# Kernel tuning notes

Measured on AMD Instinct MI355X. Metric: run time of the kernel, lower is better.

The kernel has to match this reference:

```python
import jax, jax.numpy as jnp
import numpy as np

N_QUBITS = 4
N_LAYERS = 2
_I2 = jnp.eye(2, dtype=jnp.complex64)
_X = jnp.array([[0.0, 1.0], [1.0, 0.0]], dtype=jnp.complex64)


def _apply_1q_batched(state, U, wire):
    # state: [B,2,2,2,2] complex, U: [B,2,2] (per-sample gate)
    s = jnp.moveaxis(state, 1 + wire, -1)
    s = jnp.einsum('bij,b...j->b...i', U, s)
    return jnp.moveaxis(s, -1, 1 + wire)


def _apply_1q(state, U, wire):
    # shared 2x2 gate on `wire`
    s = jnp.moveaxis(state, 1 + wire, -1)
    s = jnp.einsum('ij,...j->...i', U, s)
    return jnp.moveaxis(s, -1, 1 + wire)


def _apply_cnot(state, c, t):
    s = jnp.moveaxis(state, (1 + c, 1 + t), (-2, -1))  # [...,2(ctrl),2(tgt)]
    s = jnp.stack([s[..., 0, :], s[..., 1, ::-1]], axis=-2)  # flip target if ctrl=1
    return jnp.moveaxis(s, (-2, -1), (1 + c, 1 + t))


def _rot_matrix(phi, theta, omega):
    # qml.Rot = RZ(omega) @ RY(theta) @ RZ(phi)
    c, s = jnp.cos(theta / 2), jnp.sin(theta / 2)
    ep = jnp.exp(-0.5j * (phi + omega))  # e^{-i(phi+omega)/2}
    em = jnp.exp(-0.5j * (phi - omega))  # e^{-i(phi-omega)/2}
    return jnp.stack([
        jnp.stack([ep * c, -jnp.conj(em) * s]),
        jnp.stack([em * s, jnp.conj(ep) * c]),
    ]).astype(jnp.complex64)


def _circuit(angles, weights):
    # angles: [B, 4] real; weights: [2, 4, 3] real -> [B, 4] PauliZ expvals
    B = angles.shape[0]
    state = jnp.zeros((B,) + (2,) * N_QUBITS, jnp.complex64)
    state = state.at[(slice(None),) + (0,) * N_QUBITS].set(1.0)  # |0000>
    # AngleEmbedding (rotation='X'): RX(angle_w) on wire w, batched over samples
    for w in range(N_QUBITS):
        half = angles[:, w] / 2
        c, s = jnp.cos(half), jnp.sin(half)
        U = c[:, None, None] * _I2 - 1j * s[:, None, None] * _X  # [B,2,2]
        state = _apply_1q_batched(state, U, w)
    # StronglyEntanglingLayers: Rot on each wire, then ring of CNOTs with range r
    for l in range(N_LAYERS):
        for w in range(N_QUBITS):
            U = _rot_matrix(weights[l, w, 0], weights[l, w, 1], weights[l, w, 2])
            state = _apply_1q(state, U, w)
        r = (l % (N_QUBITS - 1)) + 1  # PennyLane default ranges
        for w in range(N_QUBITS):
            state = _apply_cnot(state, w, (w + r) % N_QUBITS)
    probs = state.real ** 2 + state.imag ** 2  # [B,2,2,2,2]
    z = []
    for w in range(N_QUBITS):
        other = tuple(a for a in range(1, N_QUBITS + 1) if a != 1 + w)
        p = probs.sum(other)  # [B,2]
        z.append(p[:, 0] - p[:, 1])
    return jnp.stack(z, axis=-1)  # [B,4]


def setup_inputs() -> dict:
    key = jax.random.key(0)
    ks = jax.random.split(key, 6)
    B, D_IN, D_OUT, NQ = 65536, 512, 512, N_QUBITS
    x = jax.random.normal(ks[0], (B, D_IN), jnp.float32)
    pre_W = jax.random.normal(ks[1], (NQ, D_IN), jnp.float32) / np.sqrt(D_IN)
    pre_b = jax.random.normal(ks[2], (NQ,), jnp.float32) * 0.05
    weights = jax.random.uniform(ks[3], (N_LAYERS, NQ, 3), jnp.float32) * (2 * np.pi)
    post_W = jax.random.normal(ks[4], (D_OUT, NQ), jnp.float32) / np.sqrt(NQ)
    post_b = jax.random.normal(ks[5], (D_OUT,), jnp.float32) * 0.05
    return {"x": x, "pre_W": pre_W, "pre_b": pre_b, "weights": weights,
            "post_W": post_W, "post_b": post_b}


def reference(x, pre_W, pre_b, weights, post_W, post_b):
    angles = jnp.tanh(x @ pre_W.T + pre_b) * jnp.pi  # [B,4]
    q = _circuit(angles, weights)                    # [B,4]
    return q @ post_W.T + post_b                     # [B,512]
```

## Files before the change

### kernel.cpp

```cpp
#include <hip/hip_runtime.h>
#include <math.h>

#define PI_F 3.14159265358979323846f


typedef float floatx4 __attribute__((ext_vector_type(4)));

static __device__ __forceinline__ void st_store4(float* p, floatx4 v)
{
    *reinterpret_cast<floatx4*>(p) = v;
}

static __device__ __forceinline__ float fast_tanh(float a)
{
    a = fminf(fmaxf(a, -15.f), 15.f);
    const float e = __expf(2.f * a);
    return (e - 1.f) / (e + 1.f);
}

template<int ST>
__device__ __forceinline__ void rot_inlane(float* ar, float* ai,
    float u00r, float u00i, float u01r, float u01i,
    float u10r, float u10i, float u11r, float u11i)
{
#pragma unroll
    for (int k = 0; k < 4; ++k) {
        if (k & ST) continue;
        const int j = k | ST;
        const float Ar = ar[k], Ai = ai[k], Br = ar[j], Bi = ai[j];
        ar[k] = u00r*Ar - u00i*Ai + u01r*Br - u01i*Bi;
        ai[k] = u00r*Ai + u00i*Ar + u01r*Bi + u01i*Br;
        ar[j] = u10r*Ar - u10i*Ai + u11r*Br - u11i*Bi;
        ai[j] = u10r*Ai + u10i*Ar + u11r*Bi + u11i*Br;
    }
}

template<int XM>
__device__ __forceinline__ void rot_cross(float* ar, float* ai, bool ownB,
    float u00r, float u00i, float u01r, float u01i,
    float u10r, float u10i, float u11r, float u11i)
{
    const float cAr = ownB ? u11r : u00r;
    const float cAi = ownB ? u11i : u00i;
    const float cBr = ownB ? u10r : u01r;
    const float cBi = ownB ? u10i : u01i;
#pragma unroll
    for (int k = 0; k < 4; ++k) {
        const float pr = __shfl_xor(ar[k], XM, 64);
        const float pi = __shfl_xor(ai[k], XM, 64);
        const float vr = ar[k], vi = ai[k];
        ar[k] = cAr*vr - cAi*vi + cBr*pr - cBi*pi;
        ai[k] = cAr*vi + cAi*vr + cBr*pi + cBi*pr;
    }
}

#define ROT_COEFFS(L, W) \
    const float ph = wts[((L)*4+(W))*3+0]; \
    const float th = wts[((L)*4+(W))*3+1]; \
    const float om = wts[((L)*4+(W))*3+2]; \
    const float s_  = __sinf(0.5f*th),        c_  = __cosf(0.5f*th); \
    const float sp_ = __sinf(0.5f*(ph+om)),   cp_ = __cosf(0.5f*(ph+om)); \
    const float sq_ = __sinf(0.5f*(ph-om)),   cq_ = __cosf(0.5f*(ph-om));

#define U_ARGS cp_*c_, -sp_*c_, -cq_*s_, -sq_*s_, cq_*s_, -sq_*s_, cp_*c_, sp_*c_

__global__ __launch_bounds__(256) void k_fused(
    const float* __restrict__ x,
    const float* __restrict__ preW,
    const float* __restrict__ preb,
    const float* __restrict__ wts,
    const float* __restrict__ postW,
    const float* __restrict__ postb,
    float* __restrict__ out, int B)
{
    const int lane  = threadIdx.x & 63;
    const int wid   = threadIdx.x >> 6;
    const int base  = blockIdx.x * 64;
    const int wbase = base + wid * 16;
    if (base >= B) return;

    __shared__ float4 angLds[64];

    float4 wA[4], wB[4];
#pragma unroll
    for (int w = 0; w < 4; ++w) {
        wA[w] = *reinterpret_cast<const float4*>(preW + w * 512 + lane * 4);
        wB[w] = *reinterpret_cast<const float4*>(preW + w * 512 + 256 + lane * 4);
    }
    const float4 pb = *reinterpret_cast<const float4*>(preb);

#pragma unroll
    for (int p = 0; p < 4; ++p) {
        const int b0 = wbase + p * 4;

        float4 xa[4], xb[4];
#pragma unroll
        for (int t = 0; t < 4; ++t) {
            const float* xr = x + (size_t)(b0 + t) * 512;
            xa[t] = *reinterpret_cast<const float4*>(xr + lane * 4);
            xb[t] = *reinterpret_cast<const float4*>(xr + 256 + lane * 4);
        }

        float acc[4][4];
#pragma unroll
        for (int t = 0; t < 4; ++t) {
#pragma unroll
            for (int w = 0; w < 4; ++w) {
                acc[t][w] = xa[t].x * wA[w].x + xa[t].y * wA[w].y + xa[t].z * wA[w].z + xa[t].w * wA[w].w
                          + xb[t].x * wB[w].x + xb[t].y * wB[w].y + xb[t].z * wB[w].z + xb[t].w * wB[w].w;
            }
        }

        float v[4];
#pragma unroll
        for (int t = 0; t < 4; ++t) {
            float a01 = (lane & 1) ? acc[t][1] : acc[t][0];
            float b01 = (lane & 1) ? acc[t][0] : acc[t][1];
            a01 += __shfl_xor(b01, 1, 64);
            float a23 = (lane & 1) ? acc[t][3] : acc[t][2];
            float b23 = (lane & 1) ? acc[t][2] : acc[t][3];
            a23 += __shfl_xor(b23, 1, 64);
            const float vv = (lane & 2) ? a23 : a01;
            const float uu = (lane & 2) ? a01 : a23;
            v[t] = vv + __shfl_xor(uu, 2, 64);
        }
        float c01 = (lane & 4) ? v[1] : v[0];
        float d01 = (lane & 4) ? v[0] : v[1];
        c01 += __shfl_xor(d01, 4, 64);
        float c23 = (lane & 4) ? v[3] : v[2];
        float d23 = (lane & 4) ? v[2] : v[3];
        c23 += __shfl_xor(d23, 4, 64);
        float m = (lane & 8) ? c23 : c01;
        float n = (lane & 8) ? c01 : c23;
        m += __shfl_xor(n, 8, 64);
        m += __shfl_xor(m, 16, 64);
        m += __shfl_xor(m, 32, 64);

        const float pb01 = (lane & 1) ? pb.y : pb.x;
        const float pb23 = (lane & 1) ? pb.w : pb.z;
        const float pbv  = (lane & 2) ? pb23 : pb01;
        const float angv = fast_tanh(m + pbv) * PI_F;

        if (lane < 16) {
            float* arow = reinterpret_cast<float*>(&angLds[wid * 16 + p * 4 + (lane >> 2)]);
            arow[lane & 3] = angv;
        }
    }

    __syncthreads();

    const int  sid = lane >> 2;
    const bool lb3 = (lane & 2) != 0;
    const bool lb2 = (lane & 1) != 0;
    const float4 ang = angLds[wid * 16 + sid];

    const float s0 = __sinf(0.5f * ang.x), c0 = __cosf(0.5f * ang.x);
    const float s1 = __sinf(0.5f * ang.y), c1 = __cosf(0.5f * ang.y);
    const float s2 = __sinf(0.5f * ang.z), c2 = __cosf(0.5f * ang.z);
    const float s3 = __sinf(0.5f * ang.w), c3 = __cosf(0.5f * ang.w);

    const float mhi = (lb3 ? s0 : c0) * (lb2 ? s1 : c1);
    const float hr  = lb3 ? (lb2 ? -mhi : 0.f) : (lb2 ? 0.f : mhi);
    const float hi  = (lb3 != lb2) ? -mhi : 0.f;
    const float low0 = c2 * c3, low1 = c2 * s3, low2 = s2 * c3, low3 = s2 * s3;

    float ar[4], ai[4];
    ar[0] =  hr * low0;  ai[0] =  hi * low0;
    ar[1] =  hi * low1;  ai[1] = -hr * low1;
    ar[2] =  hi * low2;  ai[2] = -hr * low2;
    ar[3] = -hr * low3;  ai[3] = -hi * low3;

    { ROT_COEFFS(0, 0); rot_cross<2>(ar, ai, lb3, U_ARGS); }
    { ROT_COEFFS(0, 1); rot_cross<1>(ar, ai, lb2, U_ARGS); }
    { ROT_COEFFS(0, 2); rot_inlane<2>(ar, ai, U_ARGS); }
    { ROT_COEFFS(0, 3); rot_inlane<1>(ar, ai, U_ARGS); }

    {
#pragma unroll
        for (int k = 0; k < 4; ++k) {
            const float tr = __shfl_xor(ar[k], 1, 64);
            const float ti = __shfl_xor(ai[k], 1, 64);
            ar[k] = lb3 ? tr : ar[k];
            ai[k] = lb3 ? ti : ai[k];
        }
    }
    {
        const float t0r = ar[0], t0i = ai[0], t1r = ar[1], t1i = ai[1];
        ar[0] = lb2 ? ar[2] : ar[0];  ai[0] = lb2 ? ai[2] : ai[0];
        ar[1] = lb2 ? ar[3] : ar[1];  ai[1] = lb2 ? ai[3] : ai[1];
        ar[2] = lb2 ? t0r   : ar[2];  ai[2] = lb2 ? t0i   : ai[2];
        ar[3] = lb2 ? t1r   : ar[3];  ai[3] = lb2 ? t1i   : ai[3];
    }
    {
        float t;
        t = ar[2]; ar[2] = ar[3]; ar[3] = t;
        t = ai[2]; ai[2] = ai[3]; ai[3] = t;
    }
    {
        ar[1] = __shfl_xor(ar[1], 2, 64);  ai[1] = __shfl_xor(ai[1], 2, 64);
        ar[3] = __shfl_xor(ar[3], 2, 64);  ai[3] = __shfl_xor(ai[3], 2, 64);
    }

    { ROT_COEFFS(1, 0); rot_cross<2>(ar, ai, lb3, U_ARGS); }
    { ROT_COEFFS(1, 1); rot_cross<1>(ar, ai, lb2, U_ARGS); }
    { ROT_COEFFS(1, 2); rot_inlane<2>(ar, ai, U_ARGS); }
    { ROT_COEFFS(1, 3); rot_inlane<1>(ar, ai, U_ARGS); }

    {
        const float t0r = ar[0], t0i = ai[0], t1r = ar[1], t1i = ai[1];
        ar[0] = lb3 ? ar[2] : ar[0];  ai[0] = lb3 ? ai[2] : ai[0];
        ar[1] = lb3 ? ar[3] : ar[1];  ai[1] = lb3 ? ai[3] : ai[1];
        ar[2] = lb3 ? t0r   : ar[2];  ai[2] = lb3 ? t0i   : ai[2];
        ar[3] = lb3 ? t1r   : ar[3];  ai[3] = lb3 ? t1i   : ai[3];
    }
    {
        const float t0r = ar[0], t0i = ai[0], t2r = ar[2], t2i = ai[2];
        ar[0] = lb2 ? ar[1] : ar[0];  ai[0] = lb2 ? ai[1] : ai[0];
        ar[1] = lb2 ? t0r   : ar[1];  ai[1] = lb2 ? t0i   : ai[1];
        ar[2] = lb2 ? ar[3] : ar[2];  ai[2] = lb2 ? ai[3] : ai[2];
        ar[3] = lb2 ? t2r   : ar[3];  ai[3] = lb2 ? t2i   : ai[3];
    }
    {
        ar[2] = __shfl_xor(ar[2], 2, 64);  ai[2] = __shfl_xor(ai[2], 2, 64);
        ar[3] = __shfl_xor(ar[3], 2, 64);  ai[3] = __shfl_xor(ai[3], 2, 64);
    }
    {
        ar[1] = __shfl_xor(ar[1], 1, 64);  ai[1] = __shfl_xor(ai[1], 1, 64);
        ar[3] = __shfl_xor(ar[3], 1, 64);  ai[3] = __shfl_xor(ai[3], 1, 64);
    }

    const float p0 = ar[0]*ar[0] + ai[0]*ai[0];
    const float p1 = ar[1]*ar[1] + ai[1]*ai[1];
    const float p2 = ar[2]*ar[2] + ai[2]*ai[2];
    const float p3 = ar[3]*ar[3] + ai[3]*ai[3];
    const float s01 = p0 + p1, s23 = p2 + p3;
    const float sum = s01 + s23;
    float z0 = lb3 ? -sum : sum;
    float z1 = lb2 ? -sum : sum;
    float z2 = s01 - s23;
    float z3 = (p0 - p1) + (p2 - p3);
    z0 += __shfl_xor(z0, 1, 64);  z0 += __shfl_xor(z0, 2, 64);
    z1 += __shfl_xor(z1, 1, 64);  z1 += __shfl_xor(z1, 2, 64);
    z2 += __shfl_xor(z2, 1, 64);  z2 += __shfl_xor(z2, 2, 64);
    z3 += __shfl_xor(z3, 1, 64);  z3 += __shfl_xor(z3, 2, 64);

    const float4* pW4 = reinterpret_cast<const float4*>(postW);
    const float4* pb4 = reinterpret_cast<const float4*>(postb);
    const float4 q0w = pW4[4 * lane + 0], q1w = pW4[4 * lane + 1];
    const float4 q2w = pW4[4 * lane + 2], q3w = pW4[4 * lane + 3];
    const float4 q4w = pW4[4 * (64 + lane) + 0], q5w = pW4[4 * (64 + lane) + 1];
    const float4 q6w = pW4[4 * (64 + lane) + 2], q7w = pW4[4 * (64 + lane) + 3];
    const float4 bb0 = pb4[lane], bb1 = pb4[64 + lane];

#pragma unroll
    for (int s = 0; s < 16; ++s) {
        const float q0 = __shfl(z0, s * 4, 64);
        const float q1 = __shfl(z1, s * 4, 64);
        const float q2 = __shfl(z2, s * 4, 64);
        const float q3 = __shfl(z3, s * 4, 64);
        floatx4 o0, o1;
        o0.x = fmaf(q3, q0w.w, fmaf(q2, q0w.z, fmaf(q1, q0w.y, fmaf(q0, q0w.x, bb0.x))));
        o0.y = fmaf(q3, q1w.w, fmaf(q2, q1w.z, fmaf(q1, q1w.y, fmaf(q0, q1w.x, bb0.y))));
        o0.z = fmaf(q3, q2w.w, fmaf(q2, q2w.z, fmaf(q1, q2w.y, fmaf(q0, q2w.x, bb0.z))));
        o0.w = fmaf(q3, q3w.w, fmaf(q2, q3w.z, fmaf(q1, q3w.y, fmaf(q0, q3w.x, bb0.w))));
        o1.x = fmaf(q3, q4w.w, fmaf(q2, q4w.z, fmaf(q1, q4w.y, fmaf(q0, q4w.x, bb1.x))));
        o1.y = fmaf(q3, q5w.w, fmaf(q2, q5w.z, fmaf(q1, q5w.y, fmaf(q0, q5w.x, bb1.y))));
        o1.z = fmaf(q3, q6w.w, fmaf(q2, q6w.z, fmaf(q1, q6w.y, fmaf(q0, q6w.x, bb1.z))));
        o1.w = fmaf(q3, q7w.w, fmaf(q2, q7w.z, fmaf(q1, q7w.y, fmaf(q0, q7w.x, bb1.w))));
        float* orow = out + (size_t)(wbase + s) * 512;
        st_store4(orow + 4 * lane, o0);
        st_store4(orow + 256 + 4 * lane, o1);
    }
}

extern "C" void kernel_launch(void* const* d_in, const int* in_sizes, int n_in,
                              void* d_out, int out_size, void* d_ws, size_t ws_size,
                              hipStream_t stream)
{
    const float* x     = (const float*)d_in[0];
    const float* preW  = (const float*)d_in[1];
    const float* preb  = (const float*)d_in[2];
    const float* wts   = (const float*)d_in[3];
    const float* postW = (const float*)d_in[4];
    const float* postb = (const float*)d_in[5];
    float* out = (float*)d_out;
    const int B = in_sizes[0] / 512;

    k_fused<<<dim3((B + 63) / 64), dim3(256), 0, stream>>>(
        x, preW, preb, wts, postW, postb, out, B);
}
```

Before: 46.13 us.

## Warp-specialize fused kernel into producer and consumer waves with LDS flags

```diff
diff --git a/kernel.cpp b/kernel.cpp
--- a/kernel.cpp
+++ b/kernel.cpp
@@ -5,11 +5,6 @@
 
 
 typedef float floatx4 __attribute__((ext_vector_type(4)));
-
-static __device__ __forceinline__ void st_store4(float* p, floatx4 v)
-{
-    *reinterpret_cast<floatx4*>(p) = v;
-}
 
 static __device__ __forceinline__ float fast_tanh(float a)
 {
@@ -64,7 +59,7 @@
 
 #define U_ARGS cp_*c_, -sp_*c_, -cq_*s_, -sq_*s_, cq_*s_, -sq_*s_, cp_*c_, sp_*c_
 
-__global__ __launch_bounds__(256) void k_fused(
+__global__ __launch_bounds__(512) void k_fused(
     const float* __restrict__ x,
     const float* __restrict__ preW,
     const float* __restrict__ preb,
@@ -73,203 +68,217 @@
     const float* __restrict__ postb,
     float* __restrict__ out, int B)
 {
-    const int lane  = threadIdx.x & 63;
-    const int wid   = threadIdx.x >> 6;
-    const int base  = blockIdx.x * 64;
-    const int wbase = base + wid * 16;
+    const int lane = threadIdx.x & 63;
+    const int wid  = threadIdx.x >> 6;
+    const int base = blockIdx.x * 128;
     if (base >= B) return;
 
-    __shared__ float4 angLds[64];
-
-    float4 wA[4], wB[4];
-#pragma unroll
-    for (int w = 0; w < 4; ++w) {
-        wA[w] = *reinterpret_cast<const float4*>(preW + w * 512 + lane * 4);
-        wB[w] = *reinterpret_cast<const float4*>(preW + w * 512 + 256 + lane * 4);
-    }
-    const float4 pb = *reinterpret_cast<const float4*>(preb);
-
-#pragma unroll
-    for (int p = 0; p < 4; ++p) {
-        const int b0 = wbase + p * 4;
-
-        float4 xa[4], xb[4];
-#pragma unroll
-        for (int t = 0; t < 4; ++t) {
-            const float* xr = x + (size_t)(b0 + t) * 512;
-            xa[t] = *reinterpret_cast<const float4*>(xr + lane * 4);
-            xb[t] = *reinterpret_cast<const float4*>(xr + 256 + lane * 4);
+    __shared__ float4 angLds[128];
+    __shared__ volatile int flag[8];
+    if (threadIdx.x < 8) flag[threadIdx.x] = 0;
+    __syncthreads();
+
+    if (wid < 4) {
+        const int p = wid;
+        float4 wA[4], wB[4];
+#pragma unroll
+        for (int w = 0; w < 4; ++w) {
+            wA[w] = *reinterpret_cast<const float4*>(preW + w * 512 + lane * 4);
+            wB[w] = *reinterpret_cast<const float4*>(preW + w * 512 + 256 + lane * 4);
         }
-
-        float acc[4][4];
-#pragma unroll
-        for (int t = 0; t < 4; ++t) {
-#pragma unroll
-            for (int w = 0; w < 4; ++w) {
-                acc[t][w] = xa[t].x * wA[w].x + xa[t].y * wA[w].y + xa[t].z * wA[w].z + xa[t].w * wA[w].w
-                          + xb[t].x * wB[w].x + xb[t].y * wB[w].y + xb[t].z * wB[w].z + xb[t].w * wB[w].w;
-            }
-        }
-
-        float v[4];
-#pragma unroll
-        for (int t = 0; t < 4; ++t) {
-            float a01 = (lane & 1) ? acc[t][1] : acc[t][0];
-            float b01 = (lane & 1) ? acc[t][0] : acc[t][1];
-            a01 += __shfl_xor(b01, 1, 64);
-            float a23 = (lane & 1) ? acc[t][3] : acc[t][2];
-            float b23 = (lane & 1) ? acc[t][2] : acc[t][3];
-            a23 += __shfl_xor(b23, 1, 64);
-            const float vv = (lane & 2) ? a23 : a01;
-            const float uu = (lane & 2) ? a01 : a23;
-            v[t] = vv + __shfl_xor(uu, 2, 64);
-        }
-        float c01 = (lane & 4) ? v[1] : v[0];
-        float d01 = (lane & 4) ? v[0] : v[1];
-        c01 += __shfl_xor(d01, 4, 64);
-        float c23 = (lane & 4) ? v[3] : v[2];
-        float d23 = (lane & 4) ? v[2] : v[3];
-        c23 += __shfl_xor(d23, 4, 64);
-        float m = (lane & 8) ? c23 : c01;
-        float n = (lane & 8) ? c01 : c23;
-        m += __shfl_xor(n, 8, 64);
-        m += __shfl_xor(m, 16, 64);
-        m += __shfl_xor(m, 32, 64);
-
+        const float4 pb = *reinterpret_cast<const float4*>(preb);
         const float pb01 = (lane & 1) ? pb.y : pb.x;
         const float pb23 = (lane & 1) ? pb.w : pb.z;
         const float pbv  = (lane & 2) ? pb23 : pb01;
-        const float angv = fast_tanh(m + pbv) * PI_F;
-
-        if (lane < 16) {
-            float* arow = reinterpret_cast<float*>(&angLds[wid * 16 + p * 4 + (lane >> 2)]);
-            arow[lane & 3] = angv;
+
+#pragma unroll 1
+        for (int j = 0; j < 8; ++j) {
+            const int b0 = base + 32 * p + 4 * j;
+
+            float4 xa[4], xb[4];
+#pragma unroll
+            for (int t = 0; t < 4; ++t) {
+                const float* xr = x + (size_t)(b0 + t) * 512;
+                xa[t] = *reinterpret_cast<const float4*>(xr + lane * 4);
+                xb[t] = *reinterpret_cast<const float4*>(xr + 256 + lane * 4);
+            }
+
+            float acc[4][4];
+#pragma unroll
+            for (int t = 0; t < 4; ++t) {
+#pragma unroll
+                for (int w = 0; w < 4; ++w) {
+                    acc[t][w] = xa[t].x * wA[w].x + xa[t].y * wA[w].y + xa[t].z * wA[w].z + xa[t].w * wA[w].w
+                              + xb[t].x * wB[w].x + xb[t].y * wB[w].y + xb[t].z * wB[w].z + xb[t].w * wB[w].w;
+                }
+            }
+
+            float v[4];
+#pragma unroll
+            for (int t = 0; t < 4; ++t) {
+                float a01 = (lane & 1) ? acc[t][1] : acc[t][0];
+                float b01 = (lane & 1) ? acc[t][0] : acc[t][1];
+                a01 += __shfl_xor(b01, 1, 64);
+                float a23 = (lane & 1) ? acc[t][3] : acc[t][2];
+                float b23 = (lane & 1) ? acc[t][2] : acc[t][3];
+                a23 += __shfl_xor(b23, 1, 64);
+                const float vv = (lane & 2) ? a23 : a01;
+                const float uu = (lane & 2) ? a01 : a23;
+                v[t] = vv + __shfl_xor(uu, 2, 64);
+            }
+            float c01 = (lane & 4) ? v[1] : v[0];
+            float d01 = (lane & 4) ? v[0] : v[1];
+            c01 += __shfl_xor(d01, 4, 64);
+            float c23 = (lane & 4) ? v[3] : v[2];
+            float d23 = (lane & 4) ? v[2] : v[3];
+            c23 += __shfl_xor(d23, 4, 64);
+            float m = (lane & 8) ? c23 : c01;
+            float n = (lane & 8) ? c01 : c23;
+            m += __shfl_xor(n, 8, 64);
+            m += __shfl_xor(m, 16, 64);
+            m += __shfl_xor(m, 32, 64);
+            const float angv = fast_tanh(m + pbv) * PI_F;
+
+            if (lane < 16) {
+                float* arow = reinterpret_cast<float*>(
+                    &angLds[16 * (2 * p + (j >> 2)) + 4 * (j & 3) + (lane >> 2)]);
+                arow[lane & 3] = angv;
+            }
+            if ((j & 3) == 3) {
+                __threadfence_block();
+                if (lane == 0) flag[2 * p + (j >> 2)] = 1;
+            }
         }
-    }
-
-    __syncthreads();
-
-    const int  sid = lane >> 2;
-    const bool lb3 = (lane & 2) != 0;
-    const bool lb2 = (lane & 1) != 0;
-    const float4 ang = angLds[wid * 16 + sid];
-
-    const float s0 = __sinf(0.5f * ang.x), c0 = __cosf(0.5f * ang.x);
-    const float s1 = __sinf(0.5f * ang.y), c1 = __cosf(0.5f * ang.y);
-    const float s2 = __sinf(0.5f * ang.z), c2 = __cosf(0.5f * ang.z);
-    const float s3 = __sinf(0.5f * ang.w), c3 = __cosf(0.5f * ang.w);
-
-    const float mhi = (lb3 ? s0 : c0) * (lb2 ? s1 : c1);
-    const float hr  = lb3 ? (lb2 ? -mhi : 0.f) : (lb2 ? 0.f : mhi);
-    const float hi  = (lb3 != lb2) ? -mhi : 0.f;
-    const float low0 = c2 * c3, low1 = c2 * s3, low2 = s2 * c3, low3 = s2 * s3;
-
-    float ar[4], ai[4];
-    ar[0] =  hr * low0;  ai[0] =  hi * low0;
-    ar[1] =  hi * low1;  ai[1] = -hr * low1;
-    ar[2] =  hi * low2;  ai[2] = -hr * low2;
-    ar[3] = -hr * low3;  ai[3] = -hi * low3;
-
-    { ROT_COEFFS(0, 0); rot_cross<2>(ar, ai, lb3, U_ARGS); }
-    { ROT_COEFFS(0, 1); rot_cross<1>(ar, ai, lb2, U_ARGS); }
-    { ROT_COEFFS(0, 2); rot_inlane<2>(ar, ai, U_ARGS); }
-    { ROT_COEFFS(0, 3); rot_inlane<1>(ar, ai, U_ARGS); }
-
-    {
-#pragma unroll
-        for (int k = 0; k < 4; ++k) {
-            const float tr = __shfl_xor(ar[k], 1, 64);
-            const float ti = __shfl_xor(ai[k], 1, 64);
-            ar[k] = lb3 ? tr : ar[k];
-            ai[k] = lb3 ? ti : ai[k];
+    } else {
+        const int q = wid - 4;
+        const float4* pW4 = reinterpret_cast<const float4*>(postW);
+        const float4* pb4 = reinterpret_cast<const float4*>(postb);
+        const float4 q0w = pW4[4 * lane + 0], q1w = pW4[4 * lane + 1];
+        const float4 q2w = pW4[4 * lane + 2], q3w = pW4[4 * lane + 3];
+        const float4 q4w = pW4[4 * (64 + lane) + 0], q5w = pW4[4 * (64 + lane) + 1];
+        const float4 q6w = pW4[4 * (64 + lane) + 2], q7w = pW4[4 * (64 + lane) + 3];
+        const float4 bb0 = pb4[lane], bb1 = pb4[64 + lane];
+
+        const bool lb3 = (lane & 2) != 0;
+        const bool lb2 = (lane & 1) != 0;
+        const int  sid = lane >> 2;
+
+#pragma unroll 1
+        for (int h = 0; h < 2; ++h) {
+            const int c = 2 * q + h;
+            while (flag[c] == 0) __builtin_amdgcn_s_sleep(1);
+            __threadfence_block();
+
+            const float4 ang = angLds[16 * c + sid];
+
+            const float s0 = __sinf(0.5f * ang.x), c0 = __cosf(0.5f * ang.x);
+            const float s1 = __sinf(0.5f * ang.y), c1 = __cosf(0.5f * ang.y);
+            const float s2 = __sinf(0.5f * ang.z), c2 = __cosf(0.5f * ang.z);
+            const float s3 = __sinf(0.5f * ang.w), c3 = __cosf(0.5f * ang.w);
+
+            const float mhi = (lb3 ? s0 : c0) * (lb2 ? s1 : c1);
+            const float hr  = lb3 ? (lb2 ? -mhi : 0.f) : (lb2 ? 0.f : mhi);
+            const float hi  = (lb3 != lb2) ? -mhi : 0.f;
+            const float low0 = c2 * c3, low1 = c2 * s3, low2 = s2 * c3, low3 = s2 * s3;
+
+            float ar[4], ai[4];
+            ar[0] =  hr * low0;  ai[0] =  hi * low0;
+            ar[1] =  hi * low1;  ai[1] = -hr * low1;
+            ar[2] =  hi * low2;  ai[2] = -hr * low2;
+            ar[3] = -hr * low3;  ai[3] = -hi * low3;
+
+            { ROT_COEFFS(0, 0); rot_cross<2>(ar, ai, lb3, U_ARGS); }
+            { ROT_COEFFS(0, 1); rot_cross<1>(ar, ai, lb2, U_ARGS); }
+            { ROT_COEFFS(0, 2); rot_inlane<2>(ar, ai, U_ARGS); }
+            { ROT_COEFFS(0, 3); rot_inlane<1>(ar, ai, U_ARGS); }
+            {
+#pragma unroll
+                for (int k = 0; k < 4; ++k) {
+                    const float tr = __shfl_xor(ar[k], 1, 64);
+                    const float ti = __shfl_xor(ai[k], 1, 64);
+                    ar[k] = lb3 ? tr : ar[k];
+                    ai[k] = lb3 ? ti : ai[k];
+                }
+            }
+            {
+                const float t0r = ar[0], t0i = ai[0], t1r = ar[1], t1i = ai[1];
+                ar[0] = lb2 ? ar[2] : ar[0];  ai[0] = lb2 ? ai[2] : ai[0];
+                ar[1] = lb2 ? ar[3] : ar[1];  ai[1] = lb2 ? ai[3] : ai[1];
+                ar[2] = lb2 ? t0r   : ar[2];  ai[2] = lb2 ? t0i   : ai[2];
+                ar[3] = lb2 ? t1r   : ar[3];  ai[3] = lb2 ? t1i   : ai[3];
+            }
+            {
+                float t;
+                t = ar[2]; ar[2] = ar[3]; ar[3] = t;
+                t = ai[2]; ai[2] = ai[3]; ai[3] = t;
+            }
+            {
+                ar[1] = __shfl_xor(ar[1], 2, 64);  ai[1] = __shfl_xor(ai[1], 2, 64);
+                ar[3] = __shfl_xor(ar[3], 2, 64);  ai[3] = __shfl_xor(ai[3], 2, 64);
+            }
+
+            { ROT_COEFFS(1, 0); rot_cross<2>(ar, ai, lb3, U_ARGS); }
+            { ROT_COEFFS(1, 1); rot_cross<1>(ar, ai, lb2, U_ARGS); }
+            { ROT_COEFFS(1, 2); rot_inlane<2>(ar, ai, U_ARGS); }
+            { ROT_COEFFS(1, 3); rot_inlane<1>(ar, ai, U_ARGS); }
+            {
+                const float t0r = ar[0], t0i = ai[0], t1r = ar[1], t1i = ai[1];
+                ar[0] = lb3 ? ar[2] : ar[0];  ai[0] = lb3 ? ai[2] : ai[0];
+                ar[1] = lb3 ? ar[3] : ar[1];  ai[1] = lb3 ? ai[3] : ai[1];
+                ar[2] = lb3 ? t0r   : ar[2];  ai[2] = lb3 ? t0i   : ai[2];
+                ar[3] = lb3 ? t1r   : ar[3];  ai[3] = lb3 ? t1i   : ai[3];
+            }
+            {
+                const float t0r = ar[0], t0i = ai[0], t2r = ar[2], t2i = ai[2];
+                ar[0] = lb2 ? ar[1] : ar[0];  ai[0] = lb2 ? ai[1] : ai[0];
+                ar[1] = lb2 ? t0r   : ar[1];  ai[1] = lb2 ? t0i   : ai[1];
+                ar[2] = lb2 ? ar[3] : ar[2];  ai[2] = lb2 ? ai[3] : ai[2];
+                ar[3] = lb2 ? t2r   : ar[3];  ai[3] = lb2 ? t2i   : ai[3];
+            }
+            {
+                ar[2] = __shfl_xor(ar[2], 2, 64);  ai[2] = __shfl_xor(ai[2], 2, 64);
+                ar[3] = __shfl_xor(ar[3], 2, 64);  ai[3] = __shfl_xor(ai[3], 2, 64);
+            }
+            {
+                ar[1] = __shfl_xor(ar[1], 1, 64);  ai[1] = __shfl_xor(ai[1], 1, 64);
+                ar[3] = __shfl_xor(ar[3], 1, 64);  ai[3] = __shfl_xor(ai[3], 1, 64);
+            }
+
+            const float p0 = ar[0]*ar[0] + ai[0]*ai[0];
+            const float p1 = ar[1]*ar[1] + ai[1]*ai[1];
+            const float p2 = ar[2]*ar[2] + ai[2]*ai[2];
+            const float p3 = ar[3]*ar[3] + ai[3]*ai[3];
+            const float s01 = p0 + p1, s23 = p2 + p3;
+            const float sum = s01 + s23;
+            float z0 = lb3 ? -sum : sum;
+            float z1 = lb2 ? -sum : sum;
+            float z2 = s01 - s23;
+            float z3 = (p0 - p1) + (p2 - p3);
+            z0 += __shfl_xor(z0, 1, 64);  z0 += __shfl_xor(z0, 2, 64);
+            z1 += __shfl_xor(z1, 1, 64);  z1 += __shfl_xor(z1, 2, 64);
+            z2 += __shfl_xor(z2, 1, 64);  z2 += __shfl_xor(z2, 2, 64);
+            z3 += __shfl_xor(z3, 1, 64);  z3 += __shfl_xor(z3, 2, 64);
+
+#pragma unroll
+            for (int s = 0; s < 16; ++s) {
+                const float q0 = __shfl(z0, s * 4, 64);
+                const float q1 = __shfl(z1, s * 4, 64);
+                const float q2 = __shfl(z2, s * 4, 64);
+                const float q3 = __shfl(z3, s * 4, 64);
+                floatx4 o0, o1;
+                o0.x = fmaf(q3, q0w.w, fmaf(q2, q0w.z, fmaf(q1, q0w.y, fmaf(q0, q0w.x, bb0.x))));
+                o0.y = fmaf(q3, q1w.w, fmaf(q2, q1w.z, fmaf(q1, q1w.y, fmaf(q0, q1w.x, bb0.y))));
+                o0.z = fmaf(q3, q2w.w, fmaf(q2, q2w.z, fmaf(q1, q2w.y, fmaf(q0, q2w.x, bb0.z))));
+                o0.w = fmaf(q3, q3w.w, fmaf(q2, q3w.z, fmaf(q1, q3w.y, fmaf(q0, q3w.x, bb0.w))));
+                o1.x = fmaf(q3, q4w.w, fmaf(q2, q4w.z, fmaf(q1, q4w.y, fmaf(q0, q4w.x, bb1.x))));
+                o1.y = fmaf(q3, q5w.w, fmaf(q2, q5w.z, fmaf(q1, q5w.y, fmaf(q0, q5w.x, bb1.y))));
+                o1.z = fmaf(q3, q6w.w, fmaf(q2, q6w.z, fmaf(q1, q6w.y, fmaf(q0, q6w.x, bb1.z))));
+                o1.w = fmaf(q3, q7w.w, fmaf(q2, q7w.z, fmaf(q1, q7w.y, fmaf(q0, q7w.x, bb1.w))));
+                float* orow = out + (size_t)(base + 16 * c + s) * 512;
+                *reinterpret_cast<floatx4*>(orow + 4 * lane) = o0;
+                *reinterpret_cast<floatx4*>(orow + 256 + 4 * lane) = o1;
+            }
         }
-    }
-    {
-        const float t0r = ar[0], t0i = ai[0], t1r = ar[1], t1i = ai[1];
-        ar[0] = lb2 ? ar[2] : ar[0];  ai[0] = lb2 ? ai[2] : ai[0];
-        ar[1] = lb2 ? ar[3] : ar[1];  ai[1] = lb2 ? ai[3] : ai[1];
-        ar[2] = lb2 ? t0r   : ar[2];  ai[2] = lb2 ? t0i   : ai[2];
-        ar[3] = lb2 ? t1r   : ar[3];  ai[3] = lb2 ? t1i   : ai[3];
-    }
-    {
-        float t;
-        t = ar[2]; ar[2] = ar[3]; ar[3] = t;
-        t = ai[2]; ai[2] = ai[3]; ai[3] = t;
-    }
-    {
-        ar[1] = __shfl_xor(ar[1], 2, 64);  ai[1] = __shfl_xor(ai[1], 2, 64);
-        ar[3] = __shfl_xor(ar[3], 2, 64);  ai[3] = __shfl_xor(ai[3], 2, 64);
-    }
-
-    { ROT_COEFFS(1, 0); rot_cross<2>(ar, ai, lb3, U_ARGS); }
-    { ROT_COEFFS(1, 1); rot_cross<1>(ar, ai, lb2, U_ARGS); }
-    { ROT_COEFFS(1, 2); rot_inlane<2>(ar, ai, U_ARGS); }
-    { ROT_COEFFS(1, 3); rot_inlane<1>(ar, ai, U_ARGS); }
-
-    {
-        const float t0r = ar[0], t0i = ai[0], t1r = ar[1], t1i = ai[1];
-        ar[0] = lb3 ? ar[2] : ar[0];  ai[0] = lb3 ? ai[2] : ai[0];
-        ar[1] = lb3 ? ar[3] : ar[1];  ai[1] = lb3 ? ai[3] : ai[1];
-        ar[2] = lb3 ? t0r   : ar[2];  ai[2] = lb3 ? t0i   : ai[2];
-        ar[3] = lb3 ? t1r   : ar[3];  ai[3] = lb3 ? t1i   : ai[3];
-    }
-    {
-        const float t0r = ar[0], t0i = ai[0], t2r = ar[2], t2i = ai[2];
-        ar[0] = lb2 ? ar[1] : ar[0];  ai[0] = lb2 ? ai[1] : ai[0];
-        ar[1] = lb2 ? t0r   : ar[1];  ai[1] = lb2 ? t0i   : ai[1];
-        ar[2] = lb2 ? ar[3] : ar[2];  ai[2] = lb2 ? ai[3] : ai[2];
-        ar[3] = lb2 ? t2r   : ar[3];  ai[3] = lb2 ? t2i   : ai[3];
-    }
-    {
-        ar[2] = __shfl_xor(ar[2], 2, 64);  ai[2] = __shfl_xor(ai[2], 2, 64);
-        ar[3] = __shfl_xor(ar[3], 2, 64);  ai[3] = __shfl_xor(ai[3], 2, 64);
-    }
-    {
-        ar[1] = __shfl_xor(ar[1], 1, 64);  ai[1] = __shfl_xor(ai[1], 1, 64);
-        ar[3] = __shfl_xor(ar[3], 1, 64);  ai[3] = __shfl_xor(ai[3], 1, 64);
-    }
-
-    const float p0 = ar[0]*ar[0] + ai[0]*ai[0];
-    const float p1 = ar[1]*ar[1] + ai[1]*ai[1];
-    const float p2 = ar[2]*ar[2] + ai[2]*ai[2];
-    const float p3 = ar[3]*ar[3] + ai[3]*ai[3];
-    const float s01 = p0 + p1, s23 = p2 + p3;
-    const float sum = s01 + s23;
-    float z0 = lb3 ? -sum : sum;
-    float z1 = lb2 ? -sum : sum;
-    float z2 = s01 - s23;
-    float z3 = (p0 - p1) + (p2 - p3);
-    z0 += __shfl_xor(z0, 1, 64);  z0 += __shfl_xor(z0, 2, 64);
-    z1 += __shfl_xor(z1, 1, 64);  z1 += __shfl_xor(z1, 2, 64);
-    z2 += __shfl_xor(z2, 1, 64);  z2 += __shfl_xor(z2, 2, 64);
-    z3 += __shfl_xor(z3, 1, 64);  z3 += __shfl_xor(z3, 2, 64);
-
-    const float4* pW4 = reinterpret_cast<const float4*>(postW);
-    const float4* pb4 = reinterpret_cast<const float4*>(postb);
-    const float4 q0w = pW4[4 * lane + 0], q1w = pW4[4 * lane + 1];
-    const float4 q2w = pW4[4 * lane + 2], q3w = pW4[4 * lane + 3];
-    const float4 q4w = pW4[4 * (64 + lane) + 0], q5w = pW4[4 * (64 + lane) + 1];
-    const float4 q6w = pW4[4 * (64 + lane) + 2], q7w = pW4[4 * (64 + lane) + 3];
-    const float4 bb0 = pb4[lane], bb1 = pb4[64 + lane];
-
-#pragma unroll
-    for (int s = 0; s < 16; ++s) {
-        const float q0 = __shfl(z0, s * 4, 64);
-        const float q1 = __shfl(z1, s * 4, 64);
-        const float q2 = __shfl(z2, s * 4, 64);
-        const float q3 = __shfl(z3, s * 4, 64);
-        floatx4 o0, o1;
-        o0.x = fmaf(q3, q0w.w, fmaf(q2, q0w.z, fmaf(q1, q0w.y, fmaf(q0, q0w.x, bb0.x))));
-        o0.y = fmaf(q3, q1w.w, fmaf(q2, q1w.z, fmaf(q1, q1w.y, fmaf(q0, q1w.x, bb0.y))));
-        o0.z = fmaf(q3, q2w.w, fmaf(q2, q2w.z, fmaf(q1, q2w.y, fmaf(q0, q2w.x, bb0.z))));
-        o0.w = fmaf(q3, q3w.w, fmaf(q2, q3w.z, fmaf(q1, q3w.y, fmaf(q0, q3w.x, bb0.w))));
-        o1.x = fmaf(q3, q4w.w, fmaf(q2, q4w.z, fmaf(q1, q4w.y, fmaf(q0, q4w.x, bb1.x))));
-        o1.y = fmaf(q3, q5w.w, fmaf(q2, q5w.z, fmaf(q1, q5w.y, fmaf(q0, q5w.x, bb1.y))));
-        o1.z = fmaf(q3, q6w.w, fmaf(q2, q6w.z, fmaf(q1, q6w.y, fmaf(q0, q6w.x, bb1.z))));
-        o1.w = fmaf(q3, q7w.w, fmaf(q2, q7w.z, fmaf(q1, q7w.y, fmaf(q0, q7w.x, bb1.w))));
-        float* orow = out + (size_t)(wbase + s) * 512;
-        st_store4(orow + 4 * lane, o0);
-        st_store4(orow + 256 + 4 * lane, o1);
     }
 }
 
@@ -286,6 +295,6 @@
     float* out = (float*)d_out;
     const int B = in_sizes[0] / 512;
 
-    k_fused<<<dim3((B + 63) / 64), dim3(256), 0, stream>>>(
+    k_fused<<<dim3((B + 127) / 128), dim3(512), 0, stream>>>(
         x, preW, preb, wts, postW, postb, out, B);
 }
```

Measured after the change: 46.93 us. About the same (+1.7%).
